# Kernel tuning notes

Measured on AMD Instinct MI355X. Metric: run time of the kernel, lower is better.

The kernel has to match this reference:

```python
import jax, jax.numpy as jnp
import numpy as np

B, S, D = 16, 16, 4096
H, KV, HD = 32, 8, 128
MAX_B, MAX_S = 16, 4096
START = 4080


def setup_inputs() -> dict:
    key = jax.random.key(0)
    ks = jax.random.split(key, 10)
    sc = 0.02
    # RoPE angles for positions [START, START+S)
    inv_freq = 1.0 / (10000.0 ** (np.arange(0, HD, 2, dtype=np.float32) / HD))  # [HD/2]
    pos = np.arange(START, START + S, dtype=np.float32)
    ang = np.outer(pos, inv_freq)  # [S, HD/2]
    return {
        'x': jax.random.normal(ks[0], (B, S, D), jnp.float32),
        'k': jax.random.normal(ks[1], (B, S, D), jnp.float32),
        'v': jax.random.normal(ks[2], (B, S, D), jnp.float32),
        'wq': jax.random.normal(ks[3], (D, H * HD), jnp.float32) * sc,
        'wk': jax.random.normal(ks[4], (D, KV * HD), jnp.float32) * sc,
        'wv': jax.random.normal(ks[5], (D, KV * HD), jnp.float32) * sc,
        'wo': jax.random.normal(ks[6], (H * HD, D), jnp.float32) * sc,
        'cache_k': jax.random.normal(ks[7], (MAX_B, MAX_S, KV, HD), jnp.float32),
        'cache_v': jax.random.normal(ks[8], (MAX_B, MAX_S, KV, HD), jnp.float32),
        'freqs_cos': jnp.asarray(np.cos(ang)),
        'freqs_sin': jnp.asarray(np.sin(ang)),
        'start_pos': START,
    }


def _rope(t, cos, sin):
    # t: [B,S,nh,HD]; interleaved complex pairs (even=real, odd=imag)
    t2 = t.reshape(*t.shape[:-1], HD // 2, 2)
    x0, x1 = t2[..., 0], t2[..., 1]
    c = cos[None, :, None, :]
    s = sin[None, :, None, :]
    r0 = x0 * c - x1 * s
    r1 = x0 * s + x1 * c
    return jnp.stack([r0, r1], axis=-1).reshape(t.shape)


def reference(x, k, v, wq, wk, wv, wo, cache_k, cache_v, freqs_cos, freqs_sin, start_pos):
    rep = H // KV
    xq = (x @ wq).reshape(B, S, H, HD)
    xk = (k @ wk).reshape(B, S, KV, HD)
    xv = (v @ wv).reshape(B, S, KV, HD)
    xq = _rope(xq, freqs_cos, freqs_sin)
    xk = _rope(xk, freqs_cos, freqs_sin)
    # KV-cache append (start_pos is a static Python int)
    cache_k = jax.lax.dynamic_update_slice(cache_k, xk, (0, start_pos, 0, 0))
    cache_v = jax.lax.dynamic_update_slice(cache_v, xv, (0, start_pos, 0, 0))
    T = start_pos + S
    keys = cache_k[:B, :T]    # [B,T,KV,HD]
    values = cache_v[:B, :T]  # [B,T,KV,HD]
    # GQA without materializing repeat_kv: q head h = g*rep + r
    q = xq.reshape(B, S, KV, rep, HD)
    scores = jnp.einsum('bsgrd,btgd->bgrst', q, keys) / jnp.sqrt(jnp.float32(HD))
    attn = jax.nn.softmax(scores.astype(jnp.float32), axis=-1).astype(q.dtype)
    out = jnp.einsum('bgrst,btgd->bsgrd', attn, values).reshape(B, S, H * HD)
    return out @ wo
```

## Files before the change

### kernel.cpp

```cpp
#include <hip/hip_runtime.h>

typedef __attribute__((ext_vector_type(8))) short bf8_t;
typedef __attribute__((ext_vector_type(4))) short s4_t;
typedef __attribute__((ext_vector_type(4))) float f4_t;
typedef __attribute__((ext_vector_type(4))) unsigned u4_t;

#define DEV static __device__ __forceinline__

DEV short f2bf(float f) {
  union { float f; unsigned u; } x; x.f = f;
  unsigned r = x.u + 0x7FFFu + ((x.u >> 16) & 1u);
  return (short)(r >> 16);
}
DEV float bf2f(short h) {
  union { unsigned u; float f; } x; x.u = ((unsigned)(unsigned short)h) << 16;
  return x.f;
}
DEV unsigned pk2(float a, float b) {
  return (unsigned)(unsigned short)f2bf(a) |
         ((unsigned)(unsigned short)f2bf(b) << 16);
}
DEV f4_t mfma16(bf8_t a, bf8_t b, f4_t c) {
  return __builtin_amdgcn_mfma_f32_16x16x32_bf16(a, b, c, 0, 0, 0);
}
DEV f4_t zf4() { f4_t v = {0.f, 0.f, 0.f, 0.f}; return v; }

DEV void cvt8(const f4_t& f0, const f4_t& f1, bf8_t& hv, bf8_t& lv) {
#pragma unroll
  for (int i = 0; i < 4; i++) {
    short h = f2bf(f0[i]); hv[i] = h; lv[i] = f2bf(f0[i] - bf2f(h));
  }
#pragma unroll
  for (int i = 0; i < 4; i++) {
    short h = f2bf(f1[i]); hv[4 + i] = h; lv[4 + i] = f2bf(f1[i] - bf2f(h));
  }
}

__global__ __launch_bounds__(256, 4)
void qkv_kernel(const float* __restrict__ x, const float* __restrict__ kin,
                const float* __restrict__ vin, const float* __restrict__ wq,
                const float* __restrict__ wk, const float* __restrict__ wv,
                float* __restrict__ part)
{
  __shared__ short Bh[2][64][40], Bl[2][64][40];

  int bid = blockIdx.x;
  int sw = (bid & 7) * 192 + (bid >> 3);
  int ks = sw / 384;
  int r  = sw % 384;

  int lin, N, cbase;
  const float* A; const float* W;
  if (r < 256)      { lin = r;       A = x;   W = wq; N = 4096; cbase = 0; }
  else if (r < 320) { lin = r - 256; A = kin; W = wk; N = 1024; cbase = 4096; }
  else              { lin = r - 320; A = vin; W = wv; N = 1024; cbase = 5120; }
  int m0 = (lin & 3) * 64;
  int n0 = (lin >> 2) * 64;
  int k0 = ks * 1024;

  int tid = threadIdx.x, w = tid >> 6, l = tid & 63;
  f4_t acc[4];
#pragma unroll
  for (int i = 0; i < 4; i++) acc[i] = zf4();

  int bn = tid & 63;
  int bch = (tid >> 6) ^ ((tid >> 3) & 3);
  int bk = bch * 8;
  const float* wptr = W + n0 + bn;

  const float* afrag = A + (m0 + w * 16 + (l & 15)) * 4096 + k0 + (l >> 4) * 8;

  f4_t a0 = *(const f4_t*)afrag;
  f4_t a1 = *(const f4_t*)(afrag + 4);
  float br[8];
#pragma unroll
  for (int j = 0; j < 8; j++) br[j] = wptr[(size_t)(k0 + bk + j) * N];

  for (int it = 0; it < 32; ++it) {
    int cur = it & 1;
    {
      f4_t f0, f1;
#pragma unroll
      for (int j = 0; j < 4; j++) { f0[j] = br[j]; f1[j] = br[4 + j]; }
      bf8_t hv, lv; cvt8(f0, f1, hv, lv);
      *(bf8_t*)&Bh[cur][bn][bk] = hv;
      *(bf8_t*)&Bl[cur][bn][bk] = lv;
    }
    f4_t a0c = a0, a1c = a1;
    if (it + 1 < 32) {
      a0 = *(const f4_t*)(afrag + (it + 1) * 32);
      a1 = *(const f4_t*)(afrag + (it + 1) * 32 + 4);
#pragma unroll
      for (int j = 0; j < 8; j++)
        br[j] = wptr[(size_t)(k0 + (it + 1) * 32 + bk + j) * N];
    }
    __syncthreads();
    bf8_t ah, al; cvt8(a0c, a1c, ah, al);
    __builtin_amdgcn_s_setprio(1);
#pragma unroll
    for (int nt = 0; nt < 4; ++nt) {
      bf8_t bh = *(const bf8_t*)&Bh[cur][nt * 16 + (l & 15)][(l >> 4) * 8];
      bf8_t bl = *(const bf8_t*)&Bl[cur][nt * 16 + (l & 15)][(l >> 4) * 8];
      acc[nt] = mfma16(ah, bh, acc[nt]);
      acc[nt] = mfma16(ah, bl, acc[nt]);
      acc[nt] = mfma16(al, bh, acc[nt]);
    }
    __builtin_amdgcn_s_setprio(0);
  }

  float* po = part + ((size_t)ks * 256 + m0) * 6144 + cbase + n0;
  int cl = l & 15, gq = l >> 4;
#pragma unroll
  for (int nt = 0; nt < 4; ++nt)
#pragma unroll
    for (int i = 0; i < 4; i++)
      po[(w * 16 + gq * 4 + i) * 6144 + nt * 16 + cl] = acc[nt][i];
}

__global__ __launch_bounds__(256)
void reduce_rope(const float* __restrict__ part,
                 const float* __restrict__ fcos, const float* __restrict__ fsin,
                 short* __restrict__ qh, short* __restrict__ ql,
                 float* __restrict__ kf, float* __restrict__ vf)
{
  int gid = blockIdx.x * 256 + threadIdx.x;
  int row = gid / 768;
  int c8  = (gid - row * 768) * 8;
  const float* p = part + (size_t)row * 6144 + c8;
  float v[8];
#pragma unroll
  for (int j = 0; j < 8; j++) v[j] = p[j];
#pragma unroll
  for (int ksp = 1; ksp < 4; ksp++) {
    const float* q = p + (size_t)ksp * 256 * 6144;
#pragma unroll
    for (int j = 0; j < 8; j++) v[j] += q[j];
  }
  int s = row & 15, bb = row >> 4;
  if (c8 < 4096) {
    int h = c8 >> 7, d = c8 & 127;
    f4_t c  = *(const f4_t*)(fcos + s * 64 + (d >> 1));
    f4_t sn = *(const f4_t*)(fsin + s * 64 + (d >> 1));
    bf8_t hv, lv;
#pragma unroll
    for (int pr = 0; pr < 4; pr++) {
      float x0 = v[2 * pr], x1 = v[2 * pr + 1];
      float r0 = (x0 * c[pr] - x1 * sn[pr]) * 0.08838834764831845f;
      float r1 = (x0 * sn[pr] + x1 * c[pr]) * 0.08838834764831845f;
      short h0 = f2bf(r0); hv[2 * pr] = h0; lv[2 * pr] = f2bf(r0 - bf2f(h0));
      short h1 = f2bf(r1); hv[2 * pr + 1] = h1; lv[2 * pr + 1] = f2bf(r1 - bf2f(h1));
    }
    int idx = ((bb * 8 + (h >> 2)) * 64 + (h & 3) * 16 + s) * 128 + d;
    *(bf8_t*)(qh + idx) = hv;
    *(bf8_t*)(ql + idx) = lv;
  } else if (c8 < 5120) {
    int cc = c8 - 4096; int h = cc >> 7, d = cc & 127;
    f4_t c  = *(const f4_t*)(fcos + s * 64 + (d >> 1));
    f4_t sn = *(const f4_t*)(fsin + s * 64 + (d >> 1));
    f4_t o0, o1;
#pragma unroll
    for (int pr = 0; pr < 2; pr++) {
      float x0 = v[2 * pr], x1 = v[2 * pr + 1];
      o0[2 * pr]     = x0 * c[pr] - x1 * sn[pr];
      o0[2 * pr + 1] = x0 * sn[pr] + x1 * c[pr];
    }
#pragma unroll
    for (int pr = 2; pr < 4; pr++) {
      float x0 = v[2 * pr], x1 = v[2 * pr + 1];
      o1[2 * (pr - 2)]     = x0 * c[pr] - x1 * sn[pr];
      o1[2 * (pr - 2) + 1] = x0 * sn[pr] + x1 * c[pr];
    }
    size_t idx = (((size_t)bb * 16 + s) * 8 + h) * 128 + d;
    *(f4_t*)(kf + idx) = o0;
    *(f4_t*)(kf + idx + 4) = o1;
  } else {
    int cc = c8 - 5120; int h = cc >> 7, d = cc & 127;
    size_t idx = (((size_t)bb * 16 + s) * 8 + h) * 128 + d;
    f4_t o0, o1;
#pragma unroll
    for (int j = 0; j < 4; j++) { o0[j] = v[j]; o1[j] = v[4 + j]; }
    *(f4_t*)(vf + idx) = o0;
    *(f4_t*)(vf + idx + 4) = o1;
  }
}

__global__ __launch_bounds__(256, 3)
void attn_kernel(const float* __restrict__ ck, const float* __restrict__ cv,
                 const short* __restrict__ qhp, const short* __restrict__ qlp,
                 const float* __restrict__ kfp, const float* __restrict__ vfp,
                 const int* __restrict__ startp,
                 float* __restrict__ Op, float* __restrict__ mp,
                 float* __restrict__ lp)
{
  __shared__ short Kh[32][136];
  __shared__ short Vt[128][40];
  __shared__ short Ps[4][16][40];

  int bid = blockIdx.x;
  int bg = bid >> 3, sp = bid & 7;
  int b = bg >> 3, g = bg & 7;
  int tid = threadIdx.x, w = tid >> 6, l = tid & 63;
  int start = *startp;

  bf8_t qfh[4], qfl[4];
  {
    int qoff = (bg * 64 + w * 16 + (l & 15)) * 128 + (l >> 4) * 8;
#pragma unroll
    for (int kt = 0; kt < 4; ++kt) {
      qfh[kt] = *(const bf8_t*)(qhp + qoff + kt * 32);
      qfl[kt] = *(const bf8_t*)(qlp + qoff + kt * 32);
    }
  }
  f4_t of[8];
#pragma unroll
  for (int i = 0; i < 8; i++) of[i] = zf4();
  float mrun[4], lrun[4];
#pragma unroll
  for (int i = 0; i < 4; i++) { mrun[i] = -1e30f; lrun[i] = 0.f; }

  int st_t = tid >> 3;
  int d0   = (tid & 7) * 16;
  int rr   = (tid >> 3) & 7;
  int oo   = tid >> 6;

  f4_t kr[4], vr[4];

  auto ISSUE = [&](int tile) {
    int t = sp * 512 + tile * 32 + st_t;
    size_t o_st = (((size_t)b * 4096 + t) * 8 + g) * 128;
    size_t o_fr = (((size_t)b * 16 + (size_t)(t - start)) * 8 + g) * 128;
    const float* kp_ = (t < start) ? (ck + o_st) : (kfp + o_fr);
    const float* vp_ = (t < start) ? (cv + o_st) : (vfp + o_fr);
#pragma unroll
    for (int j = 0; j < 4; j++) kr[j] = *(const f4_t*)(kp_ + d0 + 4 * j);
#pragma unroll
    for (int j = 0; j < 4; j++) vr[j] = *(const f4_t*)(vp_ + d0 + 4 * j);
  };

  auto WRITE = [&]() {
    unsigned kp[8];
#pragma unroll
    for (int p = 0; p < 8; p++)
      kp[p] = pk2(kr[p >> 1][(p & 1) * 2], kr[p >> 1][(p & 1) * 2 + 1]);
    u4_t kw0 = {kp[0], kp[1], kp[2], kp[3]};
    u4_t kw1 = {kp[4], kp[5], kp[6], kp[7]};
    *(u4_t*)&Kh[st_t][d0] = kw0;
    *(u4_t*)&Kh[st_t][d0 + 8] = kw1;

    unsigned vp[8];
#pragma unroll
    for (int p = 0; p < 8; p++)
      vp[p] = pk2(vr[p >> 1][(p & 1) * 2], vr[p >> 1][(p & 1) * 2 + 1]);
#pragma unroll
    for (int kk = 1; kk < 8; kk <<= 1) {
      unsigned nv[8];
#pragma unroll
      for (int i = 0; i < 8; i++) {
        unsigned ex = __shfl_xor(vp[i ^ kk], kk * 8);
        bool sw = (((i & kk) != 0) != ((rr & kk) != 0));
        nv[i] = sw ? ex : vp[i];
      }
#pragma unroll
      for (int i = 0; i < 8; i++) vp[i] = nv[i];
    }
    u4_t ra, rb;
#pragma unroll
    for (int i = 0; i < 4; i++) {
      ra[i] = (vp[2 * i] & 0xffffu) | (vp[2 * i + 1] << 16);
      rb[i] = (vp[2 * i] >> 16) | (vp[2 * i + 1] & 0xffff0000u);
    }
    *(u4_t*)&Vt[d0 + 2 * rr][oo * 8] = ra;
    *(u4_t*)&Vt[d0 + 2 * rr + 1][oo * 8] = rb;
  };

  ISSUE(0);
  WRITE();
  __syncthreads();
  ISSUE(1);

  for (int tile = 0; tile < 16; ++tile) {
    f4_t sf[2];
#pragma unroll
    for (int i = 0; i < 2; i++) sf[i] = zf4();
    __builtin_amdgcn_s_setprio(1);
#pragma unroll
    for (int tt = 0; tt < 2; ++tt)
#pragma unroll
      for (int kt = 0; kt < 4; ++kt) {
        bf8_t kb = *(const bf8_t*)&Kh[tt * 16 + (l & 15)][kt * 32 + (l >> 4) * 8];
        sf[tt] = mfma16(qfh[kt], kb, sf[tt]);
        sf[tt] = mfma16(qfl[kt], kb, sf[tt]);
      }
    __builtin_amdgcn_s_setprio(0);

    float mt[4];
#pragma unroll
    for (int i = 0; i < 4; i++) mt[i] = fmaxf(sf[0][i], sf[1][i]);
#pragma unroll
    for (int st = 1; st < 16; st <<= 1)
#pragma unroll
      for (int i = 0; i < 4; i++) mt[i] = fmaxf(mt[i], __shfl_xor(mt[i], st));
    float sc[4];
#pragma unroll
    for (int i = 0; i < 4; i++) {
      float mn = fmaxf(mrun[i], mt[i]);
      sc[i] = __expf(mrun[i] - mn);
      mrun[i] = mn;
    }
    float rs[4] = {0.f, 0.f, 0.f, 0.f};
#pragma unroll
    for (int tt = 0; tt < 2; ++tt)
#pragma unroll
      for (int i = 0; i < 4; i++) {
        float pexp = __expf(sf[tt][i] - mrun[i]);
        rs[i] += pexp;
        Ps[w][(l >> 4) * 4 + i][tt * 16 + (l & 15)] = f2bf(pexp);
      }
#pragma unroll
    for (int st = 1; st < 16; st <<= 1)
#pragma unroll
      for (int i = 0; i < 4; i++) rs[i] += __shfl_xor(rs[i], st);
#pragma unroll
    for (int i = 0; i < 4; i++) lrun[i] = lrun[i] * sc[i] + rs[i];
#pragma unroll
    for (int dt = 0; dt < 8; ++dt)
#pragma unroll
      for (int i = 0; i < 4; i++) of[dt][i] *= sc[i];

    __builtin_amdgcn_s_setprio(1);
    {
      bf8_t pa = *(const bf8_t*)&Ps[w][l & 15][(l >> 4) * 8];
#pragma unroll
      for (int dt = 0; dt < 8; ++dt) {
        bf8_t vfr = *(const bf8_t*)&Vt[dt * 16 + (l & 15)][(l >> 4) * 8];
        of[dt] = mfma16(pa, vfr, of[dt]);
      }
    }
    __builtin_amdgcn_s_setprio(0);

    if (tile < 15) {
      __syncthreads();
      WRITE();
      __syncthreads();
      if (tile < 14) ISSUE(tile + 2);
    }
  }

  size_t obase = ((size_t)(bg * 8 + sp) * 64 + w * 16) * 128;
#pragma unroll
  for (int dt = 0; dt < 8; ++dt)
#pragma unroll
    for (int i = 0; i < 4; i++)
      Op[obase + ((l >> 4) * 4 + i) * 128 + dt * 16 + (l & 15)] = of[dt][i];
  if ((l & 15) == 0) {
    int rbase = (bg * 8 + sp) * 64 + w * 16 + (l >> 4) * 4;
#pragma unroll
    for (int i = 0; i < 4; i++) { mp[rbase + i] = mrun[i]; lp[rbase + i] = lrun[i]; }
  }
}

__global__ __launch_bounds__(256)
void merge_kernel(const float* __restrict__ Op, const float* __restrict__ mp,
                  const float* __restrict__ lp, short* __restrict__ attnb)
{
  int bg = blockIdx.x;
  int tid = threadIdx.x;
  int row = tid >> 2, dc = (tid & 3) * 32;
  int b = bg >> 3, g = bg & 7;
  int r = row >> 4, s = row & 15;
  float mm[8], ww[8];
  float M = -1e30f;
#pragma unroll
  for (int spp = 0; spp < 8; ++spp) {
    mm[spp] = mp[(bg * 8 + spp) * 64 + row];
    M = fmaxf(M, mm[spp]);
  }
  float denom = 0.f;
#pragma unroll
  for (int spp = 0; spp < 8; ++spp) {
    ww[spp] = __expf(mm[spp] - M);
    denom += lp[(bg * 8 + spp) * 64 + row] * ww[spp];
  }
  float inv = 1.0f / denom;
  int ob = (b * 16 + s) * 4096 + (g * 4 + r) * 128 + dc;
#pragma unroll
  for (int j = 0; j < 8; j++) {
    f4_t a = zf4();
#pragma unroll
    for (int spp = 0; spp < 8; ++spp) {
      f4_t o = *(const f4_t*)(Op + ((size_t)(bg * 8 + spp) * 64 + row) * 128 + dc + j * 4);
#pragma unroll
      for (int i = 0; i < 4; i++) a[i] += ww[spp] * o[i];
    }
    s4_t o4;
#pragma unroll
    for (int i = 0; i < 4; i++) o4[i] = f2bf(a[i] * inv);
    *(s4_t*)(attnb + ob + j * 4) = o4;
  }
}

__global__ __launch_bounds__(256, 4)
void wo_kernel(const short* __restrict__ attnb, const float* __restrict__ wo,
               float* __restrict__ wpart)
{
  __shared__ short Bs[2][64][40];

  int bid = blockIdx.x;
  int sw = (bid & 7) * 128 + (bid >> 3);
  int ks = sw >> 8, r = sw & 255;
  int m0 = (r & 3) * 64, n0 = (r >> 2) * 64, k0 = ks * 1024;

  int tid = threadIdx.x, w = tid >> 6, l = tid & 63;
  f4_t acc[4];
#pragma unroll
  for (int i = 0; i < 4; i++) acc[i] = zf4();

  int bn = tid & 63;
  int bch = (tid >> 6) ^ ((tid >> 3) & 3);
  int bk = bch * 8;
  const float* wptr = wo + n0 + bn;
  const short* afrag = attnb + (m0 + w * 16 + (l & 15)) * 4096 + k0 + (l >> 4) * 8;

  bf8_t areg = *(const bf8_t*)afrag;
  float br[8];
#pragma unroll
  for (int j = 0; j < 8; j++) br[j] = wptr[(size_t)(k0 + bk + j) * 4096];

  for (int it = 0; it < 32; ++it) {
    int cur = it & 1;
    {
      bf8_t hv;
#pragma unroll
      for (int j = 0; j < 8; j++) hv[j] = f2bf(br[j]);
      *(bf8_t*)&Bs[cur][bn][bk] = hv;
    }
    bf8_t ac = areg;
    if (it + 1 < 32) {
      areg = *(const bf8_t*)(afrag + (it + 1) * 32);
#pragma unroll
      for (int j = 0; j < 8; j++)
        br[j] = wptr[(size_t)(k0 + (it + 1) * 32 + bk + j) * 4096];
    }
    __syncthreads();
    __builtin_amdgcn_s_setprio(1);
#pragma unroll
    for (int nt = 0; nt < 4; ++nt) {
      bf8_t bb_ = *(const bf8_t*)&Bs[cur][nt * 16 + (l & 15)][(l >> 4) * 8];
      acc[nt] = mfma16(ac, bb_, acc[nt]);
    }
    __builtin_amdgcn_s_setprio(0);
  }

  float* po = wpart + ((size_t)ks * 256 + m0) * 4096 + n0;
  int cl = l & 15, gq = l >> 4;
#pragma unroll
  for (int nt = 0; nt < 4; ++nt)
#pragma unroll
    for (int i = 0; i < 4; i++)
      po[(w * 16 + gq * 4 + i) * 4096 + nt * 16 + cl] = acc[nt][i];
}

__global__ __launch_bounds__(256)
void reduce_out(const float* __restrict__ wpart, float* __restrict__ out)
{
  int gid = blockIdx.x * 256 + threadIdx.x;
  size_t idx4 = (size_t)gid * 4;
  f4_t s = *(const f4_t*)(wpart + idx4);
#pragma unroll
  for (int ksp = 1; ksp < 4; ksp++) {
    f4_t t = *(const f4_t*)(wpart + (size_t)ksp * 1048576 + idx4);
#pragma unroll
    for (int i = 0; i < 4; i++) s[i] += t[i];
  }
  *(f4_t*)(out + idx4) = s;
}

extern "C" void kernel_launch(void* const* d_in, const int* in_sizes, int n_in,
                              void* d_out, int out_size, void* d_ws, size_t ws_size,
                              hipStream_t stream)
{
  const float* x  = (const float*)d_in[0];
  const float* k  = (const float*)d_in[1];
  const float* v  = (const float*)d_in[2];
  const float* wq = (const float*)d_in[3];
  const float* wk = (const float*)d_in[4];
  const float* wv = (const float*)d_in[5];
  const float* wo = (const float*)d_in[6];
  const float* ck = (const float*)d_in[7];
  const float* cv = (const float*)d_in[8];
  const float* fc = (const float*)d_in[9];
  const float* fs = (const float*)d_in[10];
  const int*   spv = (const int*)d_in[11];
  float* out = (float*)d_out;

  char* p = (char*)d_ws;
  float* S = (float*)p; p += (size_t)34 * 1024 * 1024;
  float* qpart = S;
  float* Oppp  = S;
  float* wpart = S;
  short* qh = (short*)p; p += (size_t)128 * 64 * 128 * 2;
  short* ql = (short*)p; p += (size_t)128 * 64 * 128 * 2;
  float* kf = (float*)p; p += (size_t)256 * 8 * 128 * 4;
  float* vf = (float*)p; p += (size_t)256 * 8 * 128 * 4;
  short* attnb = (short*)p; p += (size_t)256 * 4096 * 2;
  float* mp = (float*)p; p += (size_t)1024 * 64 * 4;
  float* lp = (float*)p; p += (size_t)1024 * 64 * 4;

  hipLaunchKernelGGL(qkv_kernel, dim3(1536), dim3(256), 0, stream,
                     x, k, v, wq, wk, wv, qpart);
  hipLaunchKernelGGL(reduce_rope, dim3(768), dim3(256), 0, stream,
                     qpart, fc, fs, qh, ql, kf, vf);
  hipLaunchKernelGGL(attn_kernel, dim3(1024), dim3(256), 0, stream,
                     ck, cv, qh, ql, kf, vf, spv, Oppp, mp, lp);
  hipLaunchKernelGGL(merge_kernel, dim3(128), dim3(256), 0, stream,
                     Oppp, mp, lp, attnb);
  hipLaunchKernelGGL(wo_kernel, dim3(1024), dim3(256), 0, stream,
                     attnb, wo, wpart);
  hipLaunchKernelGGL(reduce_out, dim3(1024), dim3(256), 0, stream,
                     wpart, out);
}
```

Measured before the change: 290.0 us.

## Drop split-K in QKV and Wo GEMMs, fuse RoPE/reduce epilogues, swizzle V LDS

The QKV and output projection GEMMs no longer split K four ways. Each block now computes a 32x64 tile over the full K with a two-deep register prefetch of B, and the block count drops accordingly. This lets the separate reduce_rope and reduce_out kernels be removed: RoPE, scaling and the bf16 hi/lo split are fused into the QKV epilogue using a lane shuffle, and Wo writes straight to the output. The attention kernel also XOR-swizzles the transposed V tile in LDS to reduce bank conflicts. In exchange, fewer blocks (768 and 512) run longer serial K loops, and the QKV epilogue uses scattered scalar stores.

```diff
diff --git a/kernel.cpp b/kernel.cpp
--- a/kernel.cpp
+++ b/kernel.cpp
@@ -36,151 +36,114 @@
   }
 }
 
-__global__ __launch_bounds__(256, 4)
+__global__ __launch_bounds__(256, 3)
 void qkv_kernel(const float* __restrict__ x, const float* __restrict__ kin,
                 const float* __restrict__ vin, const float* __restrict__ wq,
                 const float* __restrict__ wk, const float* __restrict__ wv,
-                float* __restrict__ part)
+                const float* __restrict__ fcos, const float* __restrict__ fsin,
+                short* __restrict__ qh, short* __restrict__ ql,
+                float* __restrict__ kf, float* __restrict__ vf)
 {
   __shared__ short Bh[2][64][40], Bl[2][64][40];
 
   int bid = blockIdx.x;
-  int sw = (bid & 7) * 192 + (bid >> 3);
-  int ks = sw / 384;
-  int r  = sw % 384;
-
-  int lin, N, cbase;
-  const float* A; const float* W;
-  if (r < 256)      { lin = r;       A = x;   W = wq; N = 4096; cbase = 0; }
-  else if (r < 320) { lin = r - 256; A = kin; W = wk; N = 1024; cbase = 4096; }
-  else              { lin = r - 320; A = vin; W = wv; N = 1024; cbase = 5120; }
-  int m0 = (lin & 3) * 64;
-  int n0 = (lin >> 2) * 64;
-  int k0 = ks * 1024;
+  int lin = (bid & 7) * 96 + (bid >> 3);
+  int m0 = (lin & 7) * 32;
+  int nglob = (lin >> 3) * 64;
+
+  int mode; int ncol0; int N; const float* A; const float* W;
+  if (nglob < 4096)      { mode = 0; A = x;   W = wq; N = 4096; ncol0 = nglob; }
+  else if (nglob < 5120) { mode = 1; A = kin; W = wk; N = 1024; ncol0 = nglob - 4096; }
+  else                   { mode = 2; A = vin; W = wv; N = 1024; ncol0 = nglob - 5120; }
 
   int tid = threadIdx.x, w = tid >> 6, l = tid & 63;
-  f4_t acc[4];
-#pragma unroll
-  for (int i = 0; i < 4; i++) acc[i] = zf4();
+  f4_t acc[2];
+#pragma unroll
+  for (int i = 0; i < 2; i++) acc[i] = zf4();
 
   int bn = tid & 63;
   int bch = (tid >> 6) ^ ((tid >> 3) & 3);
   int bk = bch * 8;
-  const float* wptr = W + n0 + bn;
-
-  const float* afrag = A + (m0 + w * 16 + (l & 15)) * 4096 + k0 + (l >> 4) * 8;
+  const float* wptr = W + ncol0 + bn;
+
+  int n32 = (w >> 1) * 32;
+  const float* afrag = A + (m0 + (w & 1) * 16 + (l & 15)) * 4096 + (l >> 4) * 8;
 
   f4_t a0 = *(const f4_t*)afrag;
   f4_t a1 = *(const f4_t*)(afrag + 4);
-  float br[8];
-#pragma unroll
-  for (int j = 0; j < 8; j++) br[j] = wptr[(size_t)(k0 + bk + j) * N];
-
-  for (int it = 0; it < 32; ++it) {
-    int cur = it & 1;
+  float brA[8], brB[8];
+#pragma unroll
+  for (int j = 0; j < 8; j++) brA[j] = wptr[(size_t)(bk + j) * N];
+#pragma unroll
+  for (int j = 0; j < 8; j++) brB[j] = wptr[(size_t)(32 + bk + j) * N];
+
+  auto body = [&](int it, float (&br)[8], int buf) {
     {
       f4_t f0, f1;
 #pragma unroll
       for (int j = 0; j < 4; j++) { f0[j] = br[j]; f1[j] = br[4 + j]; }
       bf8_t hv, lv; cvt8(f0, f1, hv, lv);
-      *(bf8_t*)&Bh[cur][bn][bk] = hv;
-      *(bf8_t*)&Bl[cur][bn][bk] = lv;
+      *(bf8_t*)&Bh[buf][bn][bk] = hv;
+      *(bf8_t*)&Bl[buf][bn][bk] = lv;
     }
     f4_t a0c = a0, a1c = a1;
-    if (it + 1 < 32) {
+    if (it + 1 < 128) {
       a0 = *(const f4_t*)(afrag + (it + 1) * 32);
       a1 = *(const f4_t*)(afrag + (it + 1) * 32 + 4);
+    }
+    if (it + 2 < 128) {
 #pragma unroll
       for (int j = 0; j < 8; j++)
-        br[j] = wptr[(size_t)(k0 + (it + 1) * 32 + bk + j) * N];
+        br[j] = wptr[(size_t)((it + 2) * 32 + bk + j) * N];
     }
     __syncthreads();
     bf8_t ah, al; cvt8(a0c, a1c, ah, al);
     __builtin_amdgcn_s_setprio(1);
 #pragma unroll
-    for (int nt = 0; nt < 4; ++nt) {
-      bf8_t bh = *(const bf8_t*)&Bh[cur][nt * 16 + (l & 15)][(l >> 4) * 8];
-      bf8_t bl = *(const bf8_t*)&Bl[cur][nt * 16 + (l & 15)][(l >> 4) * 8];
+    for (int nt = 0; nt < 2; ++nt) {
+      bf8_t bh = *(const bf8_t*)&Bh[buf][n32 + nt * 16 + (l & 15)][(l >> 4) * 8];
+      bf8_t bl = *(const bf8_t*)&Bl[buf][n32 + nt * 16 + (l & 15)][(l >> 4) * 8];
       acc[nt] = mfma16(ah, bh, acc[nt]);
       acc[nt] = mfma16(ah, bl, acc[nt]);
       acc[nt] = mfma16(al, bh, acc[nt]);
     }
     __builtin_amdgcn_s_setprio(0);
-  }
-
-  float* po = part + ((size_t)ks * 256 + m0) * 6144 + cbase + n0;
+  };
+
+  for (int p = 0; p < 64; ++p) {
+    body(2 * p,     brA, 0);
+    body(2 * p + 1, brB, 1);
+  }
+
   int cl = l & 15, gq = l >> 4;
 #pragma unroll
-  for (int nt = 0; nt < 4; ++nt)
-#pragma unroll
-    for (int i = 0; i < 4; i++)
-      po[(w * 16 + gq * 4 + i) * 6144 + nt * 16 + cl] = acc[nt][i];
-}
-
-__global__ __launch_bounds__(256)
-void reduce_rope(const float* __restrict__ part,
-                 const float* __restrict__ fcos, const float* __restrict__ fsin,
-                 short* __restrict__ qh, short* __restrict__ ql,
-                 float* __restrict__ kf, float* __restrict__ vf)
-{
-  int gid = blockIdx.x * 256 + threadIdx.x;
-  int row = gid / 768;
-  int c8  = (gid - row * 768) * 8;
-  const float* p = part + (size_t)row * 6144 + c8;
-  float v[8];
-#pragma unroll
-  for (int j = 0; j < 8; j++) v[j] = p[j];
-#pragma unroll
-  for (int ksp = 1; ksp < 4; ksp++) {
-    const float* q = p + (size_t)ksp * 256 * 6144;
-#pragma unroll
-    for (int j = 0; j < 8; j++) v[j] += q[j];
-  }
-  int s = row & 15, bb = row >> 4;
-  if (c8 < 4096) {
-    int h = c8 >> 7, d = c8 & 127;
-    f4_t c  = *(const f4_t*)(fcos + s * 64 + (d >> 1));
-    f4_t sn = *(const f4_t*)(fsin + s * 64 + (d >> 1));
-    bf8_t hv, lv;
-#pragma unroll
-    for (int pr = 0; pr < 4; pr++) {
-      float x0 = v[2 * pr], x1 = v[2 * pr + 1];
-      float r0 = (x0 * c[pr] - x1 * sn[pr]) * 0.08838834764831845f;
-      float r1 = (x0 * sn[pr] + x1 * c[pr]) * 0.08838834764831845f;
-      short h0 = f2bf(r0); hv[2 * pr] = h0; lv[2 * pr] = f2bf(r0 - bf2f(h0));
-      short h1 = f2bf(r1); hv[2 * pr + 1] = h1; lv[2 * pr + 1] = f2bf(r1 - bf2f(h1));
-    }
-    int idx = ((bb * 8 + (h >> 2)) * 64 + (h & 3) * 16 + s) * 128 + d;
-    *(bf8_t*)(qh + idx) = hv;
-    *(bf8_t*)(ql + idx) = lv;
-  } else if (c8 < 5120) {
-    int cc = c8 - 4096; int h = cc >> 7, d = cc & 127;
-    f4_t c  = *(const f4_t*)(fcos + s * 64 + (d >> 1));
-    f4_t sn = *(const f4_t*)(fsin + s * 64 + (d >> 1));
-    f4_t o0, o1;
-#pragma unroll
-    for (int pr = 0; pr < 2; pr++) {
-      float x0 = v[2 * pr], x1 = v[2 * pr + 1];
-      o0[2 * pr]     = x0 * c[pr] - x1 * sn[pr];
-      o0[2 * pr + 1] = x0 * sn[pr] + x1 * c[pr];
-    }
-#pragma unroll
-    for (int pr = 2; pr < 4; pr++) {
-      float x0 = v[2 * pr], x1 = v[2 * pr + 1];
-      o1[2 * (pr - 2)]     = x0 * c[pr] - x1 * sn[pr];
-      o1[2 * (pr - 2) + 1] = x0 * sn[pr] + x1 * c[pr];
-    }
-    size_t idx = (((size_t)bb * 16 + s) * 8 + h) * 128 + d;
-    *(f4_t*)(kf + idx) = o0;
-    *(f4_t*)(kf + idx + 4) = o1;
-  } else {
-    int cc = c8 - 5120; int h = cc >> 7, d = cc & 127;
-    size_t idx = (((size_t)bb * 16 + s) * 8 + h) * 128 + d;
-    f4_t o0, o1;
-#pragma unroll
-    for (int j = 0; j < 4; j++) { o0[j] = v[j]; o1[j] = v[4 + j]; }
-    *(f4_t*)(vf + idx) = o0;
-    *(f4_t*)(vf + idx + 4) = o1;
+  for (int nt = 0; nt < 2; ++nt) {
+    int col = nglob + n32 + nt * 16 + cl;
+#pragma unroll
+    for (int i = 0; i < 4; i++) {
+      int mrow = m0 + (w & 1) * 16 + gq * 4 + i;
+      int s = mrow & 15, bb = mrow >> 4;
+      float val = acc[nt][i];
+      if (mode == 2) {
+        int cc = col - 5120; int h = cc >> 7, d = cc & 127;
+        vf[(((size_t)bb * 16 + s) * 8 + h) * 128 + d] = val;
+      } else {
+        float other = __shfl_xor(val, 1);
+        int cc = (mode == 0) ? col : (col - 4096);
+        int d = cc & 127, h = cc >> 7;
+        float c = fcos[s * 64 + (d >> 1)], sn = fsin[s * 64 + (d >> 1)];
+        float r = ((cc & 1) == 0) ? (val * c - other * sn)
+                                  : (other * sn + val * c);
+        if (mode == 0) {
+          r *= 0.08838834764831845f;
+          short hi_ = f2bf(r), lo_ = f2bf(r - bf2f(hi_));
+          int idx = ((bb * 8 + (h >> 2)) * 64 + (h & 3) * 16 + s) * 128 + d;
+          qh[idx] = hi_; ql[idx] = lo_;
+        } else {
+          kf[(((size_t)bb * 16 + s) * 8 + h) * 128 + d] = r;
+        }
+      }
+    }
   }
 }
 
@@ -222,6 +185,7 @@
   int d0   = (tid & 7) * 16;
   int rr   = (tid >> 3) & 7;
   int oo   = tid >> 6;
+  int vunit = ((oo ^ (tid & 7)) & 3) * 8;
 
   f4_t kr[4], vr[4];
 
@@ -257,8 +221,8 @@
 #pragma unroll
       for (int i = 0; i < 8; i++) {
         unsigned ex = __shfl_xor(vp[i ^ kk], kk * 8);
-        bool sw = (((i & kk) != 0) != ((rr & kk) != 0));
-        nv[i] = sw ? ex : vp[i];
+        bool swp = (((i & kk) != 0) != ((rr & kk) != 0));
+        nv[i] = swp ? ex : vp[i];
       }
 #pragma unroll
       for (int i = 0; i < 8; i++) vp[i] = nv[i];
@@ -269,8 +233,8 @@
       ra[i] = (vp[2 * i] & 0xffffu) | (vp[2 * i + 1] << 16);
       rb[i] = (vp[2 * i] >> 16) | (vp[2 * i + 1] & 0xffff0000u);
     }
-    *(u4_t*)&Vt[d0 + 2 * rr][oo * 8] = ra;
-    *(u4_t*)&Vt[d0 + 2 * rr + 1][oo * 8] = rb;
+    *(u4_t*)&Vt[d0 + 2 * rr][vunit] = ra;
+    *(u4_t*)&Vt[d0 + 2 * rr + 1][vunit] = rb;
   };
 
   ISSUE(0);
@@ -332,7 +296,7 @@
       bf8_t pa = *(const bf8_t*)&Ps[w][l & 15][(l >> 4) * 8];
 #pragma unroll
       for (int dt = 0; dt < 8; ++dt) {
-        bf8_t vfr = *(const bf8_t*)&Vt[dt * 16 + (l & 15)][(l >> 4) * 8];
+        bf8_t vfr = *(const bf8_t*)&Vt[dt * 16 + (l & 15)][(((l >> 4) ^ dt) & 3) * 8];
         of[dt] = mfma16(pa, vfr, of[dt]);
       }
     }
@@ -399,80 +363,71 @@
   }
 }
 
-__global__ __launch_bounds__(256, 4)
+__global__ __launch_bounds__(256, 3)
 void wo_kernel(const short* __restrict__ attnb, const float* __restrict__ wo,
-               float* __restrict__ wpart)
+               float* __restrict__ out)
 {
   __shared__ short Bs[2][64][40];
 
   int bid = blockIdx.x;
-  int sw = (bid & 7) * 128 + (bid >> 3);
-  int ks = sw >> 8, r = sw & 255;
-  int m0 = (r & 3) * 64, n0 = (r >> 2) * 64, k0 = ks * 1024;
+  int lin = (bid & 7) * 64 + (bid >> 3);
+  int m0 = (lin & 7) * 32, n0 = (lin >> 3) * 64;
 
   int tid = threadIdx.x, w = tid >> 6, l = tid & 63;
-  f4_t acc[4];
-#pragma unroll
-  for (int i = 0; i < 4; i++) acc[i] = zf4();
+  f4_t acc[2];
+#pragma unroll
+  for (int i = 0; i < 2; i++) acc[i] = zf4();
 
   int bn = tid & 63;
   int bch = (tid >> 6) ^ ((tid >> 3) & 3);
   int bk = bch * 8;
   const float* wptr = wo + n0 + bn;
-  const short* afrag = attnb + (m0 + w * 16 + (l & 15)) * 4096 + k0 + (l >> 4) * 8;
+  int n32 = (w >> 1) * 32;
+  const short* afrag = attnb + (m0 + (w & 1) * 16 + (l & 15)) * 4096 + (l >> 4) * 8;
 
   bf8_t areg = *(const bf8_t*)afrag;
-  float br[8];
-#pragma unroll
-  for (int j = 0; j < 8; j++) br[j] = wptr[(size_t)(k0 + bk + j) * 4096];
-
-  for (int it = 0; it < 32; ++it) {
-    int cur = it & 1;
+  float brA[8], brB[8];
+#pragma unroll
+  for (int j = 0; j < 8; j++) brA[j] = wptr[(size_t)(bk + j) * 4096];
+#pragma unroll
+  for (int j = 0; j < 8; j++) brB[j] = wptr[(size_t)(32 + bk + j) * 4096];
+
+  auto body = [&](int it, float (&br)[8], int buf) {
     {
       bf8_t hv;
 #pragma unroll
       for (int j = 0; j < 8; j++) hv[j] = f2bf(br[j]);
-      *(bf8_t*)&Bs[cur][bn][bk] = hv;
+      *(bf8_t*)&Bs[buf][bn][bk] = hv;
     }
     bf8_t ac = areg;
-    if (it + 1 < 32) {
-      areg = *(const bf8_t*)(afrag + (it + 1) * 32);
+    if (it + 1 < 128) areg = *(const bf8_t*)(afrag + (it + 1) * 32);
+    if (it + 2 < 128) {
 #pragma unroll
       for (int j = 0; j < 8; j++)
-        br[j] = wptr[(size_t)(k0 + (it + 1) * 32 + bk + j) * 4096];
+        br[j] = wptr[(size_t)((it + 2) * 32 + bk + j) * 4096];
     }
     __syncthreads();
     __builtin_amdgcn_s_setprio(1);
 #pragma unroll
-    for (int nt = 0; nt < 4; ++nt) {
-      bf8_t bb_ = *(const bf8_t*)&Bs[cur][nt * 16 + (l & 15)][(l >> 4) * 8];
+    for (int nt = 0; nt < 2; ++nt) {
+      bf8_t bb_ = *(const bf8_t*)&Bs[buf][n32 + nt * 16 + (l & 15)][(l >> 4) * 8];
       acc[nt] = mfma16(ac, bb_, acc[nt]);
     }
     __builtin_amdgcn_s_setprio(0);
-  }
-
-  float* po = wpart + ((size_t)ks * 256 + m0) * 4096 + n0;
+  };
+
+  for (int p = 0; p < 64; ++p) {
+    body(2 * p,     brA, 0);
+    body(2 * p + 1, brB, 1);
+  }
+
   int cl = l & 15, gq = l >> 4;
 #pragma unroll
-  for (int nt = 0; nt < 4; ++nt)
+  for (int nt = 0; nt < 2; ++nt)
 #pragma unroll
     for (int i = 0; i < 4; i++)
-      po[(w * 16 + gq * 4 + i) * 4096 + nt * 16 + cl] = acc[nt][i];
-}
-
-__global__ __launch_bounds__(256)
-void reduce_out(const float* __restrict__ wpart, float* __restrict__ out)
-{
-  int gid = blockIdx.x * 256 + threadIdx.x;
-  size_t idx4 = (size_t)gid * 4;
-  f4_t s = *(const f4_t*)(wpart + idx4);
-#pragma unroll
-  for (int ksp = 1; ksp < 4; ksp++) {
-    f4_t t = *(const f4_t*)(wpart + (size_t)ksp * 1048576 + idx4);
-#pragma unroll
-    for (int i = 0; i < 4; i++) s[i] += t[i];
-  }
-  *(f4_t*)(out + idx4) = s;
+      out[(m0 + (w & 1) * 16 + gq * 4 + i) * 4096 + n0 + n32 + nt * 16 + cl] =
+          acc[nt][i];
 }
 
 extern "C" void kernel_launch(void* const* d_in, const int* in_sizes, int n_in,
@@ -494,10 +449,7 @@
   float* out = (float*)d_out;
 
   char* p = (char*)d_ws;
-  float* S = (float*)p; p += (size_t)34 * 1024 * 1024;
-  float* qpart = S;
-  float* Oppp  = S;
-  float* wpart = S;
+  float* Op = (float*)p; p += (size_t)1024 * 64 * 128 * 4;
   short* qh = (short*)p; p += (size_t)128 * 64 * 128 * 2;
   short* ql = (short*)p; p += (size_t)128 * 64 * 128 * 2;
   float* kf = (float*)p; p += (size_t)256 * 8 * 128 * 4;
@@ -506,16 +458,12 @@
   float* mp = (float*)p; p += (size_t)1024 * 64 * 4;
   float* lp = (float*)p; p += (size_t)1024 * 64 * 4;
 
-  hipLaunchKernelGGL(qkv_kernel, dim3(1536), dim3(256), 0, stream,
-                     x, k, v, wq, wk, wv, qpart);
-  hipLaunchKernelGGL(reduce_rope, dim3(768), dim3(256), 0, stream,
-                     qpart, fc, fs, qh, ql, kf, vf);
+  hipLaunchKernelGGL(qkv_kernel, dim3(768), dim3(256), 0, stream,
+                     x, k, v, wq, wk, wv, fc, fs, qh, ql, kf, vf);
   hipLaunchKernelGGL(attn_kernel, dim3(1024), dim3(256), 0, stream,
-                     ck, cv, qh, ql, kf, vf, spv, Oppp, mp, lp);
+                     ck, cv, qh, ql, kf, vf, spv, Op, mp, lp);
   hipLaunchKernelGGL(merge_kernel, dim3(128), dim3(256), 0, stream,
-                     Oppp, mp, lp, attnb);
-  hipLaunchKernelGGL(wo_kernel, dim3(1024), dim3(256), 0, stream,
-                     attnb, wo, wpart);
-  hipLaunchKernelGGL(reduce_out, dim3(1024), dim3(256), 0, stream,
-                     wpart, out);
-}
+                     Op, mp, lp, attnb);
+  hipLaunchKernelGGL(wo_kernel, dim3(512), dim3(256), 0, stream,
+                     attnb, wo, out);
+}
```

Measured after the change: 369.2 us. 1.27x slower.
